# Kernel tuning notes

Measured on AMD Instinct MI355X. Metric: run time of the kernel, lower is better.

## Reference

```python
import jax, jax.numpy as jnp
import numpy as np
from math import factorial, comb

N_NODES = 50000
N_EDGES = 640000
FEAT = 32
NUM_BASIS = 8
CUTOFF = 5.0
MAX_Z = 118
NUM_ITERS = 3
LMAX = 2
K = (LMAX + 1) ** 2  # 9 spherical channels for max_degree=2


def _assoc_legendre(c, s, lmax):
    # associated Legendre P_l^m without Condon-Shortley phase
    P = {(0, 0): np.ones_like(c)}
    for m in range(1, lmax + 1):
        P[(m, m)] = P[(m - 1, m - 1)] * (2 * m - 1) * s
    for m in range(lmax):
        P[(m + 1, m)] = (2 * m + 1) * c * P[(m, m)]
    for m in range(lmax + 1):
        for l in range(m + 2, lmax + 1):
            P[(l, m)] = ((2 * l - 1) * c * P[(l - 1, m)] - (l + m - 1) * P[(l - 2, m)]) / (l - m)
    return P


def _real_sh_np(xyz, lmax):
    # Racah-normalized real spherical harmonics (Y_00 = 1), order m=-l..l
    r = np.linalg.norm(xyz, axis=1)
    cth = xyz[:, 2] / r
    sth = np.sqrt(np.maximum(1.0 - cth ** 2, 0.0))
    phi = np.arctan2(xyz[:, 1], xyz[:, 0])
    P = _assoc_legendre(cth, sth, lmax)
    cols = []
    for l in range(lmax + 1):
        for m in range(-l, l + 1):
            am = abs(m)
            if m == 0:
                cols.append(P[(l, 0)])
            else:
                nrm = np.sqrt(2.0 * factorial(l - am) / factorial(l + am))
                ang = np.cos(am * phi) if m > 0 else np.sin(am * phi)
                cols.append(nrm * P[(l, am)] * ang)
    return np.stack(cols, axis=1)


def _gaunt_tensor():
    # cg[k1,k2,k3]: expansion of Y_k1 * Y_k2 onto Y_k3 (degrees <= 2).
    # Products of degree<=2 harmonics lie exactly in span of degree<=4 harmonics,
    # so the least-squares fit below recovers exact coefficients.
    rng = np.random.default_rng(0)
    pts = rng.normal(size=(4096, 3))
    pts /= np.linalg.norm(pts, axis=1, keepdims=True)
    A = _real_sh_np(pts, 2 * LMAX)  # (M, 25)
    Y = A[:, :K]                    # (M, 9)
    prod = (Y[:, :, None] * Y[:, None, :]).reshape(len(pts), K * K)
    coef, *_ = np.linalg.lstsq(A, prod, rcond=None)  # (25, 81)
    return coef[:K].reshape(K, K, K).transpose(1, 2, 0).astype(np.float32)


CG = jnp.asarray(_gaunt_tensor())  # (9, 9, 9)
LOG_BINOM = jnp.asarray([np.log(comb(NUM_BASIS - 1, kk)) for kk in range(NUM_BASIS)], dtype=jnp.float32)


def _sh_l2(u):
    # Racah real SH of unit vectors, degrees 0..2, order m=-l..l
    x, y, z = u[:, 0], u[:, 1], u[:, 2]
    s3 = 1.7320508075688772
    return jnp.stack([
        jnp.ones_like(x),
        y, z, x,
        s3 * x * y, s3 * y * z, 0.5 * (3.0 * z * z - 1.0), s3 * x * z, 0.5 * s3 * (x * x - y * y),
    ], axis=1)


def _radial(r):
    # reciprocal Bernstein basis (log-space, stable) * smooth cutoff
    u = r / (1.0 + r)
    k = jnp.arange(NUM_BASIS, dtype=jnp.float32)
    n = float(NUM_BASIS - 1)
    eps = 1e-12
    logu = jnp.log(jnp.maximum(u, eps))[:, None]
    log1u = jnp.log(jnp.maximum(1.0 - u, eps))[:, None]
    bern = jnp.exp(LOG_BINOM + k * logu + (n - k) * log1u)  # (E, B)
    cut = jnp.where(r < CUTOFF, jnp.exp(-(r * r) / jnp.maximum(CUTOFF * CUTOFF - r * r, eps)), 0.0)
    return bern * cut[:, None]


def _forward(dr_vec, embed, rad_w, d1w, d1b, d2w, d2b, Z, neighbor_idxs):
    idx_i, idx_j = neighbor_idxs[0], neighbor_idxs[1]
    r = jnp.linalg.norm(dr_vec, axis=1)
    u = dr_vec / jnp.maximum(r, 1e-9)[:, None]
    Ysh = _sh_l2(u)              # (E, 9) angular basis
    rad = _radial(r)             # (E, B) radial basis
    # mask padding edges (idx_i == idx_j) as in mask_by_neighbor
    rad = rad * (idx_i != idx_j).astype(rad.dtype)[:, None]

    N = Z.shape[0]
    x = jnp.zeros((N, K, FEAT), jnp.float32).at[:, 0, :].set(embed[Z])

    for i in range(NUM_ITERS):
        last = i == NUM_ITERS - 1
        k3 = 1 if last else K    # last MessagePass has max_degree=0
        xe = x[idx_j]                                  # (E, 9, F) edge gather
        g = jnp.einsum('eb,dbf->edf', rad, rad_w[i])   # (E, 3, F) radial->feature per basis degree
        y = jnp.zeros((N_EDGES, k3, FEAT), jnp.float32)
        for l2 in range(LMAX + 1):
            sl = slice(l2 * l2, (l2 + 1) ** 2)
            c = jnp.einsum('abc,eb->eac', CG[:, sl, :k3], Ysh[:, sl])          # (E, 9, k3)
            y = y + jnp.einsum('eac,eaf->ecf', c, xe * g[:, l2][:, None, :])   # (E, k3, F)
        m = jax.ops.segment_sum(y, idx_i, num_segments=N)                      # scatter-sum
        if last:
            x = x[:, :1, :]      # change_max_degree_or_type(x, 0)
        h = x + m
        h = jnp.einsum('nkf,fg->nkg', h, d1w[i]).at[:, 0, :].add(d1b[i])
        gate = jax.nn.sigmoid(h[:, :1, :])
        h = h * gate             # silu on scalar channel, sigmoid-gated tensor channels
        h = jnp.einsum('nkf,fg->nkg', h, d2w[i]).at[:, 0, :].add(d2b[i])
        x = x + h
    return x[:, 0, :]            # (N, F)


def setup_inputs() -> dict:
    key = jax.random.key(0)
    ks = jax.random.split(key, 8)
    dr_vec = jax.random.normal(ks[0], (N_EDGES, 3), jnp.float32) * 2.0
    Z = jax.random.randint(ks[1], (N_NODES,), 0, MAX_Z + 1, jnp.int32)
    neighbor_idxs = jax.random.randint(ks[2], (2, N_EDGES), 0, N_NODES, jnp.int32)
    embed = jax.random.normal(ks[3], (MAX_Z + 1, FEAT), jnp.float32)
    rad_w = jax.random.normal(ks[4], (NUM_ITERS, LMAX + 1, NUM_BASIS, FEAT), jnp.float32) * 0.5
    d1w = jax.random.normal(ks[5], (NUM_ITERS, FEAT, FEAT), jnp.float32) * (1.0 / np.sqrt(FEAT))
    d1b = jnp.zeros((NUM_ITERS, FEAT), jnp.float32)
    d2w = jax.random.normal(ks[6], (NUM_ITERS, FEAT, FEAT), jnp.float32) * 0.02
    d2b = jnp.zeros((NUM_ITERS, FEAT), jnp.float32)
    return {"dr_vec": dr_vec, "embed": embed, "rad_w": rad_w, "d1w": d1w, "d1b": d1b,
            "d2w": d2w, "d2b": d2b, "Z": Z, "neighbor_idxs": neighbor_idxs}


def reference(dr_vec, embed, rad_w, d1w, d1b, d2w, d2b, Z, neighbor_idxs):
    return _forward(dr_vec, embed, rad_w, d1w, d1b, d2w, d2b, Z, neighbor_idxs)
```

## Files before the change

### kernel.cpp

```cpp
#include <hip/hip_runtime.h>
#include <hip/hip_fp16.h>
#include <math.h>

#define NN 50000
#define NE 640000
#define F  32
#define KCH 9
#define CUT 5.0f

#define C13 (1.0f/3.0f)
#define C23 (2.0f/3.0f)
#define C15 0.2f
#define C25 0.4f
#define C17 (1.0f/7.0f)
#define C27 (2.0f/7.0f)
#define IS3 0.5773502691896258f
#define S35 0.3464101615137755f
#define S37 0.2474358296526968f
#define S3  1.7320508075688772f

union U2H { unsigned int u; __half2 h; };

__device__ __forceinline__ unsigned int pack2(float a, float b) {
    U2H c; c.h = __floats2half2_rn(a, b); return c.u;
}
__device__ __forceinline__ float2 unpack2(unsigned int u) {
    U2H c; c.u = u; return __half22float2(c.h);
}
__device__ __forceinline__ float h2f(ushort u) {
    return __half2float(__ushort_as_half(u));
}

__global__ __launch_bounds__(256) void init_x(const float* __restrict__ embed,
                                              const int* __restrict__ Z,
                                              float* __restrict__ x0,
                                              ushort* __restrict__ x0h,
                                              uint4* __restrict__ xhA,
                                              ushort* __restrict__ xhB) {
    int idx = blockIdx.x * 256 + threadIdx.x;
    int n = idx >> 5, f = idx & 31;
    float v = embed[Z[n] * F + f];
    x0[idx] = v;
    unsigned int p = pack2(v, 0.f);
    x0h[idx] = (ushort)(p & 0xFFFFu);
    uint4 ua; ua.x = p; ua.y = 0u; ua.z = 0u; ua.w = 0u;
    xhA[idx] = ua;
    xhB[idx] = 0;
}

__global__ __launch_bounds__(256) void hist_kernel(const int* __restrict__ idx_i,
                                                   const int* __restrict__ idx_j,
                                                   const float* __restrict__ dr,
                                                   int* __restrict__ cnt) {
    int e = blockIdx.x * 256 + threadIdx.x;
    if (e >= NE) return;
    int ni = idx_i[e], nj = idx_j[e];
    float dx = dr[3 * e + 0], dy = dr[3 * e + 1], dz = dr[3 * e + 2];
    float r2 = fmaf(dx, dx, fmaf(dy, dy, dz * dz));
    if (ni != nj && r2 < CUT * CUT) atomicAdd(&cnt[ni], 1);
}

#define SCAN_T 1024
#define SCAN_C ((NN + SCAN_T - 1) / SCAN_T)

__global__ __launch_bounds__(SCAN_T) void scan_kernel(const int* __restrict__ cnt,
                                                      int* __restrict__ offs,
                                                      int* __restrict__ head) {
    __shared__ int ps[SCAN_T];
    int t = threadIdx.x;
    int b = t * SCAN_C;
    int e = min(b + SCAN_C, NN);
    int s = 0;
    for (int i = b; i < e; ++i) s += cnt[i];
    ps[t] = s;
    __syncthreads();
    for (int off = 1; off < SCAN_T; off <<= 1) {
        int v = (t >= off) ? ps[t - off] : 0;
        __syncthreads();
        ps[t] += v;
        __syncthreads();
    }
    int run = (t == 0) ? 0 : ps[t - 1];
    for (int i = b; i < e; ++i) { int c = cnt[i]; offs[i] = run; head[i] = run; run += c; }
    if (t == SCAN_T - 1) offs[NN] = ps[SCAN_T - 1];
}

__global__ __launch_bounds__(256) void fill_kernel(const int* __restrict__ idx_i,
                                                   const int* __restrict__ idx_j,
                                                   const float* __restrict__ dr,
                                                   int* __restrict__ head,
                                                   uint2* __restrict__ erec) {
    int e = blockIdx.x * 256 + threadIdx.x;
    if (e >= NE) return;
    int ni = idx_i[e], nj = idx_j[e];
    float dx = dr[3 * e + 0], dy = dr[3 * e + 1], dz = dr[3 * e + 2];
    float r2 = fmaf(dx, dx, fmaf(dy, dy, dz * dz));
    if (!(ni != nj && r2 < CUT * CUT)) return;

    float r = sqrtf(r2);
    float inv = 1.0f / fmaxf(r, 1e-9f);
    float ux = dx * inv, uy = dy * inv, uz = dz * inv;

    float cut = expf(-r2 / fmaxf(CUT * CUT - r2, 1e-12f));
    float ur = r / (1.0f + r), vr = 1.0f - ur;
    float up2 = ur*ur, up3 = up2*ur, up4 = up3*ur, up5 = up4*ur, up6 = up5*ur, up7 = up6*ur;
    float vp2 = vr*vr, vp3 = vp2*vr, vp4 = vp3*vr, vp5 = vp4*vr, vp6 = vp5*vr, vp7 = vp6*vr;

    float rc0 = cut * vp7;
    float rc1 = cut * 7.f  * ur  * vp6;
    float rc2 = cut * 21.f * up2 * vp5;
    float rc3 = cut * 35.f * up3 * vp4;
    float rc4 = cut * 35.f * up4 * vp3;
    float rc5 = cut * 21.f * up5 * vp2;
    float rc6 = cut * 7.f  * up6 * vr;
    float rc7 = cut * up7;

    int p = atomicAdd(&head[ni], 1);
    uint2 e0, e1, e2;
    U2H zh; zh.h = __floats2half2_rn(uz, 0.f);
    e0.x = pack2(ux, uy);
    e0.y = (zh.u & 0xFFFFu) | ((unsigned int)nj << 16);
    e1.x = pack2(rc0, rc1); e1.y = pack2(rc2, rc3);
    e2.x = pack2(rc4, rc5); e2.y = pack2(rc6, rc7);
    erec[(size_t)3 * p + 0] = e0;
    erec[(size_t)3 * p + 1] = e1;
    erec[(size_t)3 * p + 2] = e2;
}

template<int MODE>
__global__ __launch_bounds__(256) void gather_kernel(const uint2* __restrict__ erec,
                                                     const ushort* __restrict__ x0h,
                                                     const uint4* __restrict__ xhA,
                                                     const ushort* __restrict__ xhB,
                                                     const float* __restrict__ rw_iter,
                                                     const int* __restrict__ offs,
                                                     float* __restrict__ m) {
    const int NWAVES = 2048 * 4;
    int lane = threadIdx.x & 63;
    int wid  = threadIdx.x >> 6;
    int half = lane >> 5;
    int f    = lane & 31;
    int gw   = blockIdx.x * 4 + wid;

    float rwv[24];
    #pragma unroll
    for (int lb = 0; lb < 24; ++lb) rwv[lb] = rw_iter[lb * F + f];
    if (MODE == 2) {
        #pragma unroll
        for (int lb = 8; lb < 16; ++lb) rwv[lb] *= C13;
        #pragma unroll
        for (int lb = 16; lb < 24; ++lb) rwv[lb] *= C15;
    }

    constexpr int NACC = (MODE == 2) ? 1 : KCH;

    for (int n = gw; n < NN; n += NWAVES) {
        int start = offs[n], end = offs[n + 1];

        float acc[NACC];
        #pragma unroll
        for (int a = 0; a < NACC; ++a) acc[a] = 0.f;

        int t = start + half;
        uint2 e0_0 = {}, e0_1 = {}, e0_2 = {};
        uint4 xa_0 = {}, xa_1 = {};
        ushort x8_0 = 0, x8_1 = 0;

        if (t < end) {
            int c1 = min(t + 2, end - 1);
            int c2 = min(t + 4, end - 1);
            e0_0 = erec[(size_t)3 * t];
            e0_1 = erec[(size_t)3 * c1];
            e0_2 = erec[(size_t)3 * c2];
            int nj0 = (int)(e0_0.y >> 16);
            int nj1 = (int)(e0_1.y >> 16);
            if (MODE == 0) {
                x8_0 = x0h[nj0 * F + f];
                x8_1 = x0h[nj1 * F + f];
            } else {
                xa_0 = xhA[nj0 * F + f]; x8_0 = xhB[nj0 * F + f];
                xa_1 = xhA[nj1 * F + f]; x8_1 = xhB[nj1 * F + f];
            }
        }

        while (t < end) {
            uint2 e1 = erec[(size_t)3 * t + 1];
            uint2 e2 = erec[(size_t)3 * t + 2];

            int c3 = min(t + 6, end - 1);
            uint2 e0_3 = erec[(size_t)3 * c3];
            int nj2 = (int)(e0_2.y >> 16);
            uint4 xa_2 = {};
            ushort x8_2;
            if (MODE == 0) {
                x8_2 = x0h[nj2 * F + f];
            } else {
                xa_2 = xhA[nj2 * F + f];
                x8_2 = xhB[nj2 * F + f];
            }

            float2 uxy = unpack2(e0_0.x);
            float ux = uxy.x, uy = uxy.y;
            float uz = unpack2(e0_0.y).x;
            float2 rcA = unpack2(e1.x);
            float2 rcB = unpack2(e1.y);
            float2 rcC = unpack2(e2.x);
            float2 rcD = unpack2(e2.y);

            float g0, g1, g2;
            g0 = rcA.x * rwv[0];
            g0 = fmaf(rcA.y, rwv[1], g0); g0 = fmaf(rcB.x, rwv[2], g0); g0 = fmaf(rcB.y, rwv[3], g0);
            g0 = fmaf(rcC.x, rwv[4], g0); g0 = fmaf(rcC.y, rwv[5], g0); g0 = fmaf(rcD.x, rwv[6], g0);
            g0 = fmaf(rcD.y, rwv[7], g0);
            g1 = rcA.x * rwv[8];
            g1 = fmaf(rcA.y, rwv[9],  g1); g1 = fmaf(rcB.x, rwv[10], g1); g1 = fmaf(rcB.y, rwv[11], g1);
            g1 = fmaf(rcC.x, rwv[12], g1); g1 = fmaf(rcC.y, rwv[13], g1); g1 = fmaf(rcD.x, rwv[14], g1);
            g1 = fmaf(rcD.y, rwv[15], g1);
            g2 = rcA.x * rwv[16];
            g2 = fmaf(rcA.y, rwv[17], g2); g2 = fmaf(rcB.x, rwv[18], g2); g2 = fmaf(rcB.y, rwv[19], g2);
            g2 = fmaf(rcC.x, rwv[20], g2); g2 = fmaf(rcC.y, rwv[21], g2); g2 = fmaf(rcD.x, rwv[22], g2);
            g2 = fmaf(rcD.y, rwv[23], g2);

            if (MODE == 0) {
                float xe0 = h2f(x8_0);
                float s2 = S3 * g2;
                acc[0] = fmaf(xe0, g0, acc[0]);
                acc[1] = fmaf(xe0, uy * g1, acc[1]);
                acc[2] = fmaf(xe0, uz * g1, acc[2]);
                acc[3] = fmaf(xe0, ux * g1, acc[3]);
                acc[4] = fmaf(xe0, s2 * ux * uy, acc[4]);
                acc[5] = fmaf(xe0, s2 * uy * uz, acc[5]);
                acc[6] = fmaf(xe0, fmaf(1.5f * uz, uz, -0.5f) * g2, acc[6]);
                acc[7] = fmaf(xe0, s2 * ux * uz, acc[7]);
                acc[8] = fmaf(xe0, 0.5f * s2 * (ux * ux - uy * uy), acc[8]);
            } else {
                float xe[9];
                {
                    float2 p;
                    p = unpack2(xa_0.x); xe[0] = p.x; xe[1] = p.y;
                    p = unpack2(xa_0.y); xe[2] = p.x; xe[3] = p.y;
                    p = unpack2(xa_0.z); xe[4] = p.x; xe[5] = p.y;
                    p = unpack2(xa_0.w); xe[6] = p.x; xe[7] = p.y;
                    xe[8] = h2f(x8_0);
                }
                if (MODE == 2) {
                    float dot1 = uy * xe[1];
                    dot1 = fmaf(uz, xe[2], dot1);
                    dot1 = fmaf(ux, xe[3], dot1);
                    float Y4 = S3 * ux * uy, Y5 = S3 * uy * uz, Y7 = S3 * ux * uz;
                    float Y6 = fmaf(1.5f * uz, uz, -0.5f);
                    float Y8 = 0.5f * S3 * (ux * ux - uy * uy);
                    float dot2 = Y4 * xe[4];
                    dot2 = fmaf(Y5, xe[5], dot2);
                    dot2 = fmaf(Y6, xe[6], dot2);
                    dot2 = fmaf(Y7, xe[7], dot2);
                    dot2 = fmaf(Y8, xe[8], dot2);
                    acc[0] = fmaf(g0, xe[0], acc[0]);
                    acc[0] = fmaf(g1, dot1, acc[0]);
                    acc[0] = fmaf(g2, dot2, acc[0]);
                } else {
                    float s2 = S3 * g2;
                    float w[9];
                    w[0] = g0;
                    w[1] = uy * g1; w[2] = uz * g1; w[3] = ux * g1;
                    w[4] = s2 * ux * uy;
                    w[5] = s2 * uy * uz;
                    w[6] = fmaf(1.5f * uz, uz, -0.5f) * g2;
                    w[7] = s2 * ux * uz;
                    w[8] = 0.5f * s2 * (ux * ux - uy * uy);

                    float d0 = xe[0]*w[0], d1 = xe[1]*w[1], d2 = xe[2]*w[2], d3 = xe[3]*w[3];
                    float d4 = xe[4]*w[4], d5 = xe[5]*w[5], d6 = xe[6]*w[6], d7 = xe[7]*w[7];
                    float d8 = xe[8]*w[8];

                    acc[0] += d0 + C13 * (d1 + d2 + d3) + C15 * (d4 + d5 + d6 + d7 + d8);
                    #define T(a, b) (xe[a] * w[b] + xe[b] * w[a])
                    acc[1] += T(0,1) - C15 * T(1,6) - S35 * T(1,8) + S35 * T(2,5) + S35 * T(3,4);
                    acc[2] += T(0,2) + S35 * T(1,5) + C25 * T(2,6) + S35 * T(3,7);
                    acc[3] += T(0,3) + S35 * T(1,4) + S35 * T(2,7) - C15 * T(3,6) + S35 * T(3,8);
                    acc[4] += T(0,4) + IS3 * T(1,3) - C27 * T(4,6) + S37 * T(5,7);
                    acc[5] += T(0,5) + IS3 * T(1,2) + S37 * T(4,7) + C17 * T(5,6) - S37 * T(5,8);
                    acc[6] += T(0,6) - C13 * d1 + C23 * d2 - C13 * d3
                            - C27 * d4 + C17 * d5 + C27 * d6 + C17 * d7 - C27 * d8;
                    acc[7] += T(0,7) + IS3 * T(2,3) + S37 * T(4,5) + C17 * T(6,7) + S37 * T(7,8);
                    acc[8] += T(0,8) - IS3 * d1 + IS3 * d3 - S37 * d5 + S37 * d7 - C27 * T(6,8);
                    #undef T
                }
            }

            e0_0 = e0_1; e0_1 = e0_2; e0_2 = e0_3;
            xa_0 = xa_1; xa_1 = xa_2;
            x8_0 = x8_1; x8_1 = x8_2;
            t += 2;
        }

        #pragma unroll
        for (int a = 0; a < NACC; ++a) acc[a] += __shfl_xor(acc[a], 32);

        if (half == 0) {
            if (MODE == 2) {
                m[(size_t)n * F + f] = acc[0];
            } else {
                float* mp = m + (size_t)n * KCH * F + f;
                #pragma unroll
                for (int a = 0; a < KCH; ++a) mp[a * F] = acc[a];
            }
        }
    }
}

__global__ __launch_bounds__(256) void node_full(float* __restrict__ x0,
                                                 const float* __restrict__ m,
                                                 uint4* __restrict__ xhA,
                                                 ushort* __restrict__ xhB,
                                                 const float* __restrict__ w1,
                                                 const float* __restrict__ b1,
                                                 const float* __restrict__ w2,
                                                 const float* __restrict__ b2) {
    __shared__ float tile[8][KCH][F];
    int nl = threadIdx.x >> 5, f = threadIdx.x & 31;
    int n = blockIdx.x * 8 + nl;

    float w1c[F];
    #pragma unroll
    for (int fi = 0; fi < F; ++fi) w1c[fi] = w1[fi * F + f];

    float xk[KCH];
    {
        uint4 ua = xhA[n * F + f];
        ushort ub = xhB[n * F + f];
        float2 p;
        p = unpack2(ua.x); xk[0] = p.x; xk[1] = p.y;
        p = unpack2(ua.y); xk[2] = p.x; xk[3] = p.y;
        p = unpack2(ua.z); xk[4] = p.x; xk[5] = p.y;
        p = unpack2(ua.w); xk[6] = p.x; xk[7] = p.y;
        xk[8] = h2f(ub);
    }
    xk[0] = x0[n * F + f];

    #pragma unroll
    for (int k = 0; k < KCH; ++k)
        tile[nl][k][f] = xk[k] + m[((size_t)n * KCH + k) * F + f];
    __syncthreads();

    float o1[KCH];
    #pragma unroll
    for (int k = 0; k < KCH; ++k) {
        float s = 0.f;
        #pragma unroll
        for (int fi = 0; fi < F; ++fi) s = fmaf(tile[nl][k][fi], w1c[fi], s);
        o1[k] = s;
    }
    o1[0] += b1[f];
    float gate = 1.0f / (1.0f + expf(-o1[0]));
    __syncthreads();
    #pragma unroll
    for (int k = 0; k < KCH; ++k) tile[nl][k][f] = o1[k] * gate;
    __syncthreads();

    float w2c[F];
    #pragma unroll
    for (int fi = 0; fi < F; ++fi) w2c[fi] = w2[fi * F + f];

    float xn[KCH];
    #pragma unroll
    for (int k = 0; k < KCH; ++k) {
        float s = (k == 0) ? b2[f] : 0.f;
        #pragma unroll
        for (int fi = 0; fi < F; ++fi) s = fmaf(tile[nl][k][fi], w2c[fi], s);
        xn[k] = xk[k] + s;
    }

    x0[n * F + f] = xn[0];
    uint4 ua;
    ua.x = pack2(xn[0], xn[1]); ua.y = pack2(xn[2], xn[3]);
    ua.z = pack2(xn[4], xn[5]); ua.w = pack2(xn[6], xn[7]);
    xhA[n * F + f] = ua;
    xhB[n * F + f] = __half_as_ushort(__float2half_rn(xn[8]));
}

__global__ __launch_bounds__(256) void node_last(const float* __restrict__ x0,
                                                 const float* __restrict__ m1,
                                                 const float* __restrict__ w1,
                                                 const float* __restrict__ b1,
                                                 const float* __restrict__ w2,
                                                 const float* __restrict__ b2,
                                                 float* __restrict__ out) {
    __shared__ float tile[8][F];
    int nl = threadIdx.x >> 5, f = threadIdx.x & 31;
    int n = blockIdx.x * 8 + nl;

    float w1c[F];
    #pragma unroll
    for (int fi = 0; fi < F; ++fi) w1c[fi] = w1[fi * F + f];

    float xv = x0[n * F + f];
    tile[nl][f] = xv + m1[(size_t)n * F + f];
    __syncthreads();
    float s = 0.f;
    #pragma unroll
    for (int fi = 0; fi < F; ++fi) s = fmaf(tile[nl][fi], w1c[fi], s);
    s += b1[f];
    float gate = 1.0f / (1.0f + expf(-s));
    float h2 = s * gate;
    __syncthreads();
    tile[nl][f] = h2;
    __syncthreads();
    float w2c[F];
    #pragma unroll
    for (int fi = 0; fi < F; ++fi) w2c[fi] = w2[fi * F + f];
    float o = b2[f];
    #pragma unroll
    for (int fi = 0; fi < F; ++fi) o = fmaf(tile[nl][fi], w2c[fi], o);
    out[(size_t)n * F + f] = xv + o;
}

extern "C" void kernel_launch(void* const* d_in, const int* in_sizes, int n_in,
                              void* d_out, int out_size, void* d_ws, size_t ws_size,
                              hipStream_t stream) {
    (void)in_sizes; (void)n_in; (void)out_size; (void)ws_size;
    const float* dr    = (const float*)d_in[0];
    const float* embed = (const float*)d_in[1];
    const float* rad_w = (const float*)d_in[2];
    const float* d1w   = (const float*)d_in[3];
    const float* d1b   = (const float*)d_in[4];
    const float* d2w   = (const float*)d_in[5];
    const float* d2b   = (const float*)d_in[6];
    const int*   Z     = (const int*)d_in[7];
    const int*   nidx  = (const int*)d_in[8];
    const int* idx_i = nidx;
    const int* idx_j = nidx + NE;

    uint4* xhA = (uint4*)d_ws;
    float* m   = (float*)(xhA + (size_t)NN * F);
    float* x0  = m + (size_t)NN * KCH * F;
    ushort* x0h = (ushort*)(x0 + (size_t)NN * F);
    ushort* xhB = x0h + (size_t)NN * F;
    uint2* erec = (uint2*)(xhB + (size_t)NN * F);
    int* offs = (int*)(erec + (size_t)3 * NE);
    int* head = offs + (NN + 1);
    int* cnt  = head + NN;
    float* outp = (float*)d_out;

    hipMemsetAsync(cnt, 0, NN * sizeof(int), stream);
    hist_kernel<<<(NE + 255) / 256, 256, 0, stream>>>(idx_i, idx_j, dr, cnt);
    scan_kernel<<<1, SCAN_T, 0, stream>>>(cnt, offs, head);
    fill_kernel<<<(NE + 255) / 256, 256, 0, stream>>>(idx_i, idx_j, dr, head, erec);

    init_x<<<NN * F / 256, 256, 0, stream>>>(embed, Z, x0, x0h, xhA, xhB);

    for (int i = 0; i < 3; ++i) {
        const float* rwi = rad_w + (size_t)i * 3 * 8 * F;
        const float* w1 = d1w + (size_t)i * F * F;
        const float* b1 = d1b + (size_t)i * F;
        const float* w2 = d2w + (size_t)i * F * F;
        const float* b2 = d2b + (size_t)i * F;
        if (i == 0) {
            gather_kernel<0><<<2048, 256, 0, stream>>>(erec, x0h, xhA, xhB, rwi, offs, m);
            node_full<<<NN / 8, 256, 0, stream>>>(x0, m, xhA, xhB, w1, b1, w2, b2);
        } else if (i == 1) {
            gather_kernel<1><<<2048, 256, 0, stream>>>(erec, x0h, xhA, xhB, rwi, offs, m);
            node_full<<<NN / 8, 256, 0, stream>>>(x0, m, xhA, xhB, w1, b1, w2, b2);
        } else {
            gather_kernel<2><<<2048, 256, 0, stream>>>(erec, x0h, xhA, xhB, rwi, offs, m);
            node_last<<<NN / 8, 256, 0, stream>>>(x0, m, w1, b1, w2, b2, outp);
        }
    }
}
```

Measured before the change: 571.2 us.

## Split gather work into equal edge ranges with segmented atomic flushes

The gather kernel no longer assigns one node per wave. Each half-wave now takes an equal contiguous slice of the sorted edge list, accumulates per destination node, and flushes partial sums with float atomics whenever the destination changes. Edge records are repacked from three uint2 reads into a uint4 plus uint2 per edge, with a separate 16-bit destination array. The message buffer is zeroed before each iteration. The aim is even load balance and no idle lanes on low-degree nodes, paid for by an extra memset and atomic traffic at segment boundaries.

```diff
diff --git a/kernel.cpp b/kernel.cpp
--- a/kernel.cpp
+++ b/kernel.cpp
@@ -19,6 +19,9 @@
 #define S37 0.2474358296526968f
 #define S3  1.7320508075688772f
 
+#define NBLK 2048
+#define NHALF (NBLK * 8)
+
 union U2H { unsigned int u; __half2 h; };
 
 __device__ __forceinline__ unsigned int pack2(float a, float b) {
@@ -38,8 +41,8 @@
                                               uint4* __restrict__ xhA,
                                               ushort* __restrict__ xhB) {
     int idx = blockIdx.x * 256 + threadIdx.x;
-    int n = idx >> 5, f = idx & 31;
-    float v = embed[Z[n] * F + f];
+    int n = idx >> 5;
+    float v = embed[Z[n] * F + (idx & 31)];
     x0[idx] = v;
     unsigned int p = pack2(v, 0.f);
     x0h[idx] = (ushort)(p & 0xFFFFu);
@@ -89,7 +92,9 @@
                                                    const int* __restrict__ idx_j,
                                                    const float* __restrict__ dr,
                                                    int* __restrict__ head,
-                                                   uint2* __restrict__ erec) {
+                                                   uint4* __restrict__ geoA,
+                                                   uint2* __restrict__ geoB,
+                                                   ushort* __restrict__ dstA) {
     int e = blockIdx.x * 256 + threadIdx.x;
     if (e >= NE) return;
     int ni = idx_i[e], nj = idx_j[e];
@@ -106,41 +111,36 @@
     float up2 = ur*ur, up3 = up2*ur, up4 = up3*ur, up5 = up4*ur, up6 = up5*ur, up7 = up6*ur;
     float vp2 = vr*vr, vp3 = vp2*vr, vp4 = vp3*vr, vp5 = vp4*vr, vp6 = vp5*vr, vp7 = vp6*vr;
 
-    float rc0 = cut * vp7;
-    float rc1 = cut * 7.f  * ur  * vp6;
-    float rc2 = cut * 21.f * up2 * vp5;
-    float rc3 = cut * 35.f * up3 * vp4;
-    float rc4 = cut * 35.f * up4 * vp3;
-    float rc5 = cut * 21.f * up5 * vp2;
-    float rc6 = cut * 7.f  * up6 * vr;
-    float rc7 = cut * up7;
-
     int p = atomicAdd(&head[ni], 1);
-    uint2 e0, e1, e2;
+    uint4 gA;
     U2H zh; zh.h = __floats2half2_rn(uz, 0.f);
-    e0.x = pack2(ux, uy);
-    e0.y = (zh.u & 0xFFFFu) | ((unsigned int)nj << 16);
-    e1.x = pack2(rc0, rc1); e1.y = pack2(rc2, rc3);
-    e2.x = pack2(rc4, rc5); e2.y = pack2(rc6, rc7);
-    erec[(size_t)3 * p + 0] = e0;
-    erec[(size_t)3 * p + 1] = e1;
-    erec[(size_t)3 * p + 2] = e2;
+    gA.x = pack2(ux, uy);
+    gA.y = (zh.u & 0xFFFFu) | ((unsigned int)nj << 16);
+    gA.z = pack2(cut * vp7,        cut * 7.f  * ur  * vp6);
+    gA.w = pack2(cut * 21.f * up2 * vp5, cut * 35.f * up3 * vp4);
+    uint2 gB;
+    gB.x = pack2(cut * 35.f * up4 * vp3, cut * 21.f * up5 * vp2);
+    gB.y = pack2(cut * 7.f  * up6 * vr,  cut * up7);
+    geoA[p] = gA;
+    geoB[p] = gB;
+    dstA[p] = (ushort)ni;
 }
 
 template<int MODE>
-__global__ __launch_bounds__(256) void gather_kernel(const uint2* __restrict__ erec,
+__global__ __launch_bounds__(256) void gather_kernel(const uint4* __restrict__ geoA,
+                                                     const uint2* __restrict__ geoB,
+                                                     const ushort* __restrict__ dstA,
                                                      const ushort* __restrict__ x0h,
                                                      const uint4* __restrict__ xhA,
                                                      const ushort* __restrict__ xhB,
                                                      const float* __restrict__ rw_iter,
-                                                     const int* __restrict__ offs,
+                                                     const int* __restrict__ neptr,
                                                      float* __restrict__ m) {
-    const int NWAVES = 2048 * 4;
     int lane = threadIdx.x & 63;
     int wid  = threadIdx.x >> 6;
     int half = lane >> 5;
     int f    = lane & 31;
-    int gw   = blockIdx.x * 4 + wid;
+    int h    = blockIdx.x * 8 + wid * 2 + half;
 
     float rwv[24];
     #pragma unroll
@@ -152,159 +152,167 @@
         for (int lb = 16; lb < 24; ++lb) rwv[lb] *= C15;
     }
 
+    int NEl = neptr[0];
+    int per = (NEl + NHALF - 1) / NHALF;
+    int s = h * per;
+    int e = min(s + per, NEl);
+    if (s >= e) return;
+
     constexpr int NACC = (MODE == 2) ? 1 : KCH;
-
-    for (int n = gw; n < NN; n += NWAVES) {
-        int start = offs[n], end = offs[n + 1];
-
-        float acc[NACC];
-        #pragma unroll
-        for (int a = 0; a < NACC; ++a) acc[a] = 0.f;
-
-        int t = start + half;
-        uint2 e0_0 = {}, e0_1 = {}, e0_2 = {};
-        uint4 xa_0 = {}, xa_1 = {};
-        ushort x8_0 = 0, x8_1 = 0;
-
-        if (t < end) {
-            int c1 = min(t + 2, end - 1);
-            int c2 = min(t + 4, end - 1);
-            e0_0 = erec[(size_t)3 * t];
-            e0_1 = erec[(size_t)3 * c1];
-            e0_2 = erec[(size_t)3 * c2];
-            int nj0 = (int)(e0_0.y >> 16);
-            int nj1 = (int)(e0_1.y >> 16);
-            if (MODE == 0) {
-                x8_0 = x0h[nj0 * F + f];
-                x8_1 = x0h[nj1 * F + f];
+    float acc[NACC];
+    #pragma unroll
+    for (int a = 0; a < NACC; ++a) acc[a] = 0.f;
+    int cur = -1;
+
+    int c1 = min(s + 1, e - 1), c2 = min(s + 2, e - 1);
+    uint4 gA0 = geoA[s], gA1 = geoA[c1], gA2 = geoA[c2];
+    uint2 gB0 = geoB[s], gB1 = geoB[c1];
+    int d0 = dstA[s], d1 = dstA[c1];
+    int nj0 = (int)(gA0.y >> 16), nj1 = (int)(gA1.y >> 16);
+    uint4 xa0 = {}, xa1 = {};
+    ushort x80, x81;
+    if (MODE == 0) {
+        x80 = x0h[nj0 * F + f];
+        x81 = x0h[nj1 * F + f];
+    } else {
+        xa0 = xhA[nj0 * F + f]; x80 = xhB[nj0 * F + f];
+        xa1 = xhA[nj1 * F + f]; x81 = xhB[nj1 * F + f];
+    }
+
+    for (int t = s; t < e; ++t) {
+        int t3 = min(t + 3, e - 1);
+        int t2 = min(t + 2, e - 1);
+        uint4 gA3 = geoA[t3];
+        uint2 gB2 = geoB[t2];
+        int d2 = dstA[t2];
+        int nj2 = (int)(gA2.y >> 16);
+        uint4 xa2 = {};
+        ushort x82;
+        if (MODE == 0) {
+            x82 = x0h[nj2 * F + f];
+        } else {
+            xa2 = xhA[nj2 * F + f];
+            x82 = xhB[nj2 * F + f];
+        }
+
+        if (d0 != cur) {
+            if (cur >= 0) {
+                if (MODE == 2) {
+                    unsafeAtomicAdd(m + (size_t)cur * F + f, acc[0]);
+                } else {
+                    float* mp = m + (size_t)cur * KCH * F + f;
+                    #pragma unroll
+                    for (int a = 0; a < KCH; ++a) unsafeAtomicAdd(mp + a * F, acc[a]);
+                }
+            }
+            cur = d0;
+            #pragma unroll
+            for (int a = 0; a < NACC; ++a) acc[a] = 0.f;
+        }
+
+        float2 uxy = unpack2(gA0.x);
+        float ux = uxy.x, uy = uxy.y;
+        float uz = unpack2(gA0.y).x;
+        float2 rcA = unpack2(gA0.z);
+        float2 rcB = unpack2(gA0.w);
+        float2 rcC = unpack2(gB0.x);
+        float2 rcD = unpack2(gB0.y);
+
+        float g0, g1, g2;
+        g0 = rcA.x * rwv[0];
+        g0 = fmaf(rcA.y, rwv[1], g0); g0 = fmaf(rcB.x, rwv[2], g0); g0 = fmaf(rcB.y, rwv[3], g0);
+        g0 = fmaf(rcC.x, rwv[4], g0); g0 = fmaf(rcC.y, rwv[5], g0); g0 = fmaf(rcD.x, rwv[6], g0);
+        g0 = fmaf(rcD.y, rwv[7], g0);
+        g1 = rcA.x * rwv[8];
+        g1 = fmaf(rcA.y, rwv[9],  g1); g1 = fmaf(rcB.x, rwv[10], g1); g1 = fmaf(rcB.y, rwv[11], g1);
+        g1 = fmaf(rcC.x, rwv[12], g1); g1 = fmaf(rcC.y, rwv[13], g1); g1 = fmaf(rcD.x, rwv[14], g1);
+        g1 = fmaf(rcD.y, rwv[15], g1);
+        g2 = rcA.x * rwv[16];
+        g2 = fmaf(rcA.y, rwv[17], g2); g2 = fmaf(rcB.x, rwv[18], g2); g2 = fmaf(rcB.y, rwv[19], g2);
+        g2 = fmaf(rcC.x, rwv[20], g2); g2 = fmaf(rcC.y, rwv[21], g2); g2 = fmaf(rcD.x, rwv[22], g2);
+        g2 = fmaf(rcD.y, rwv[23], g2);
+
+        if (MODE == 0) {
+            float xe0 = h2f(x80);
+            float s2 = S3 * g2;
+            acc[0] = fmaf(xe0, g0, acc[0]);
+            acc[1] = fmaf(xe0, uy * g1, acc[1]);
+            acc[2] = fmaf(xe0, uz * g1, acc[2]);
+            acc[3] = fmaf(xe0, ux * g1, acc[3]);
+            acc[4] = fmaf(xe0, s2 * ux * uy, acc[4]);
+            acc[5] = fmaf(xe0, s2 * uy * uz, acc[5]);
+            acc[6] = fmaf(xe0, fmaf(1.5f * uz, uz, -0.5f) * g2, acc[6]);
+            acc[7] = fmaf(xe0, s2 * ux * uz, acc[7]);
+            acc[8] = fmaf(xe0, 0.5f * s2 * (ux * ux - uy * uy), acc[8]);
+        } else {
+            float xe[9];
+            {
+                float2 p;
+                p = unpack2(xa0.x); xe[0] = p.x; xe[1] = p.y;
+                p = unpack2(xa0.y); xe[2] = p.x; xe[3] = p.y;
+                p = unpack2(xa0.z); xe[4] = p.x; xe[5] = p.y;
+                p = unpack2(xa0.w); xe[6] = p.x; xe[7] = p.y;
+                xe[8] = h2f(x80);
+            }
+            if (MODE == 2) {
+                float dot1 = uy * xe[1];
+                dot1 = fmaf(uz, xe[2], dot1);
+                dot1 = fmaf(ux, xe[3], dot1);
+                float Y4 = S3 * ux * uy, Y5 = S3 * uy * uz, Y7 = S3 * ux * uz;
+                float Y6 = fmaf(1.5f * uz, uz, -0.5f);
+                float Y8 = 0.5f * S3 * (ux * ux - uy * uy);
+                float dot2 = Y4 * xe[4];
+                dot2 = fmaf(Y5, xe[5], dot2);
+                dot2 = fmaf(Y6, xe[6], dot2);
+                dot2 = fmaf(Y7, xe[7], dot2);
+                dot2 = fmaf(Y8, xe[8], dot2);
+                acc[0] = fmaf(g0, xe[0], acc[0]);
+                acc[0] = fmaf(g1, dot1, acc[0]);
+                acc[0] = fmaf(g2, dot2, acc[0]);
             } else {
-                xa_0 = xhA[nj0 * F + f]; x8_0 = xhB[nj0 * F + f];
-                xa_1 = xhA[nj1 * F + f]; x8_1 = xhB[nj1 * F + f];
+                float s2 = S3 * g2;
+                float w[9];
+                w[0] = g0;
+                w[1] = uy * g1; w[2] = uz * g1; w[3] = ux * g1;
+                w[4] = s2 * ux * uy;
+                w[5] = s2 * uy * uz;
+                w[6] = fmaf(1.5f * uz, uz, -0.5f) * g2;
+                w[7] = s2 * ux * uz;
+                w[8] = 0.5f * s2 * (ux * ux - uy * uy);
+
+                float d0v = xe[0]*w[0], d1v = xe[1]*w[1], d2v = xe[2]*w[2], d3v = xe[3]*w[3];
+                float d4v = xe[4]*w[4], d5v = xe[5]*w[5], d6v = xe[6]*w[6], d7v = xe[7]*w[7];
+                float d8v = xe[8]*w[8];
+
+                acc[0] += d0v + C13 * (d1v + d2v + d3v) + C15 * (d4v + d5v + d6v + d7v + d8v);
+                #define T(a, b) (xe[a] * w[b] + xe[b] * w[a])
+                acc[1] += T(0,1) - C15 * T(1,6) - S35 * T(1,8) + S35 * T(2,5) + S35 * T(3,4);
+                acc[2] += T(0,2) + S35 * T(1,5) + C25 * T(2,6) + S35 * T(3,7);
+                acc[3] += T(0,3) + S35 * T(1,4) + S35 * T(2,7) - C15 * T(3,6) + S35 * T(3,8);
+                acc[4] += T(0,4) + IS3 * T(1,3) - C27 * T(4,6) + S37 * T(5,7);
+                acc[5] += T(0,5) + IS3 * T(1,2) + S37 * T(4,7) + C17 * T(5,6) - S37 * T(5,8);
+                acc[6] += T(0,6) - C13 * d1v + C23 * d2v - C13 * d3v
+                        - C27 * d4v + C17 * d5v + C27 * d6v + C17 * d7v - C27 * d8v;
+                acc[7] += T(0,7) + IS3 * T(2,3) + S37 * T(4,5) + C17 * T(6,7) + S37 * T(7,8);
+                acc[8] += T(0,8) - IS3 * d1v + IS3 * d3v - S37 * d5v + S37 * d7v - C27 * T(6,8);
+                #undef T
             }
         }
 
-        while (t < end) {
-            uint2 e1 = erec[(size_t)3 * t + 1];
-            uint2 e2 = erec[(size_t)3 * t + 2];
-
-            int c3 = min(t + 6, end - 1);
-            uint2 e0_3 = erec[(size_t)3 * c3];
-            int nj2 = (int)(e0_2.y >> 16);
-            uint4 xa_2 = {};
-            ushort x8_2;
-            if (MODE == 0) {
-                x8_2 = x0h[nj2 * F + f];
-            } else {
-                xa_2 = xhA[nj2 * F + f];
-                x8_2 = xhB[nj2 * F + f];
-            }
-
-            float2 uxy = unpack2(e0_0.x);
-            float ux = uxy.x, uy = uxy.y;
-            float uz = unpack2(e0_0.y).x;
-            float2 rcA = unpack2(e1.x);
-            float2 rcB = unpack2(e1.y);
-            float2 rcC = unpack2(e2.x);
-            float2 rcD = unpack2(e2.y);
-
-            float g0, g1, g2;
-            g0 = rcA.x * rwv[0];
-            g0 = fmaf(rcA.y, rwv[1], g0); g0 = fmaf(rcB.x, rwv[2], g0); g0 = fmaf(rcB.y, rwv[3], g0);
-            g0 = fmaf(rcC.x, rwv[4], g0); g0 = fmaf(rcC.y, rwv[5], g0); g0 = fmaf(rcD.x, rwv[6], g0);
-            g0 = fmaf(rcD.y, rwv[7], g0);
-            g1 = rcA.x * rwv[8];
-            g1 = fmaf(rcA.y, rwv[9],  g1); g1 = fmaf(rcB.x, rwv[10], g1); g1 = fmaf(rcB.y, rwv[11], g1);
-            g1 = fmaf(rcC.x, rwv[12], g1); g1 = fmaf(rcC.y, rwv[13], g1); g1 = fmaf(rcD.x, rwv[14], g1);
-            g1 = fmaf(rcD.y, rwv[15], g1);
-            g2 = rcA.x * rwv[16];
-            g2 = fmaf(rcA.y, rwv[17], g2); g2 = fmaf(rcB.x, rwv[18], g2); g2 = fmaf(rcB.y, rwv[19], g2);
-            g2 = fmaf(rcC.x, rwv[20], g2); g2 = fmaf(rcC.y, rwv[21], g2); g2 = fmaf(rcD.x, rwv[22], g2);
-            g2 = fmaf(rcD.y, rwv[23], g2);
-
-            if (MODE == 0) {
-                float xe0 = h2f(x8_0);
-                float s2 = S3 * g2;
-                acc[0] = fmaf(xe0, g0, acc[0]);
-                acc[1] = fmaf(xe0, uy * g1, acc[1]);
-                acc[2] = fmaf(xe0, uz * g1, acc[2]);
-                acc[3] = fmaf(xe0, ux * g1, acc[3]);
-                acc[4] = fmaf(xe0, s2 * ux * uy, acc[4]);
-                acc[5] = fmaf(xe0, s2 * uy * uz, acc[5]);
-                acc[6] = fmaf(xe0, fmaf(1.5f * uz, uz, -0.5f) * g2, acc[6]);
-                acc[7] = fmaf(xe0, s2 * ux * uz, acc[7]);
-                acc[8] = fmaf(xe0, 0.5f * s2 * (ux * ux - uy * uy), acc[8]);
-            } else {
-                float xe[9];
-                {
-                    float2 p;
-                    p = unpack2(xa_0.x); xe[0] = p.x; xe[1] = p.y;
-                    p = unpack2(xa_0.y); xe[2] = p.x; xe[3] = p.y;
-                    p = unpack2(xa_0.z); xe[4] = p.x; xe[5] = p.y;
-                    p = unpack2(xa_0.w); xe[6] = p.x; xe[7] = p.y;
-                    xe[8] = h2f(x8_0);
-                }
-                if (MODE == 2) {
-                    float dot1 = uy * xe[1];
-                    dot1 = fmaf(uz, xe[2], dot1);
-                    dot1 = fmaf(ux, xe[3], dot1);
-                    float Y4 = S3 * ux * uy, Y5 = S3 * uy * uz, Y7 = S3 * ux * uz;
-                    float Y6 = fmaf(1.5f * uz, uz, -0.5f);
-                    float Y8 = 0.5f * S3 * (ux * ux - uy * uy);
-                    float dot2 = Y4 * xe[4];
-                    dot2 = fmaf(Y5, xe[5], dot2);
-                    dot2 = fmaf(Y6, xe[6], dot2);
-                    dot2 = fmaf(Y7, xe[7], dot2);
-                    dot2 = fmaf(Y8, xe[8], dot2);
-                    acc[0] = fmaf(g0, xe[0], acc[0]);
-                    acc[0] = fmaf(g1, dot1, acc[0]);
-                    acc[0] = fmaf(g2, dot2, acc[0]);
-                } else {
-                    float s2 = S3 * g2;
-                    float w[9];
-                    w[0] = g0;
-                    w[1] = uy * g1; w[2] = uz * g1; w[3] = ux * g1;
-                    w[4] = s2 * ux * uy;
-                    w[5] = s2 * uy * uz;
-                    w[6] = fmaf(1.5f * uz, uz, -0.5f) * g2;
-                    w[7] = s2 * ux * uz;
-                    w[8] = 0.5f * s2 * (ux * ux - uy * uy);
-
-                    float d0 = xe[0]*w[0], d1 = xe[1]*w[1], d2 = xe[2]*w[2], d3 = xe[3]*w[3];
-                    float d4 = xe[4]*w[4], d5 = xe[5]*w[5], d6 = xe[6]*w[6], d7 = xe[7]*w[7];
-                    float d8 = xe[8]*w[8];
-
-                    acc[0] += d0 + C13 * (d1 + d2 + d3) + C15 * (d4 + d5 + d6 + d7 + d8);
-                    #define T(a, b) (xe[a] * w[b] + xe[b] * w[a])
-                    acc[1] += T(0,1) - C15 * T(1,6) - S35 * T(1,8) + S35 * T(2,5) + S35 * T(3,4);
-                    acc[2] += T(0,2) + S35 * T(1,5) + C25 * T(2,6) + S35 * T(3,7);
-                    acc[3] += T(0,3) + S35 * T(1,4) + S35 * T(2,7) - C15 * T(3,6) + S35 * T(3,8);
-                    acc[4] += T(0,4) + IS3 * T(1,3) - C27 * T(4,6) + S37 * T(5,7);
-                    acc[5] += T(0,5) + IS3 * T(1,2) + S37 * T(4,7) + C17 * T(5,6) - S37 * T(5,8);
-                    acc[6] += T(0,6) - C13 * d1 + C23 * d2 - C13 * d3
-                            - C27 * d4 + C17 * d5 + C27 * d6 + C17 * d7 - C27 * d8;
-                    acc[7] += T(0,7) + IS3 * T(2,3) + S37 * T(4,5) + C17 * T(6,7) + S37 * T(7,8);
-                    acc[8] += T(0,8) - IS3 * d1 + IS3 * d3 - S37 * d5 + S37 * d7 - C27 * T(6,8);
-                    #undef T
-                }
-            }
-
-            e0_0 = e0_1; e0_1 = e0_2; e0_2 = e0_3;
-            xa_0 = xa_1; xa_1 = xa_2;
-            x8_0 = x8_1; x8_1 = x8_2;
-            t += 2;
-        }
-
-        #pragma unroll
-        for (int a = 0; a < NACC; ++a) acc[a] += __shfl_xor(acc[a], 32);
-
-        if (half == 0) {
-            if (MODE == 2) {
-                m[(size_t)n * F + f] = acc[0];
-            } else {
-                float* mp = m + (size_t)n * KCH * F + f;
-                #pragma unroll
-                for (int a = 0; a < KCH; ++a) mp[a * F] = acc[a];
-            }
+        gA0 = gA1; gA1 = gA2; gA2 = gA3;
+        gB0 = gB1; gB1 = gB2;
+        d0 = d1; d1 = d2;
+        xa0 = xa1; xa1 = xa2;
+        x80 = x81; x81 = x82;
+    }
+
+    if (cur >= 0) {
+        if (MODE == 2) {
+            unsafeAtomicAdd(m + (size_t)cur * F + f, acc[0]);
+        } else {
+            float* mp = m + (size_t)cur * KCH * F + f;
+            #pragma unroll
+            for (int a = 0; a < KCH; ++a) unsafeAtomicAdd(mp + a * F, acc[a]);
         }
     }
 }
@@ -431,24 +439,30 @@
     const int* idx_i = nidx;
     const int* idx_j = nidx + NE;
 
-    uint4* xhA = (uint4*)d_ws;
-    float* m   = (float*)(xhA + (size_t)NN * F);
-    float* x0  = m + (size_t)NN * KCH * F;
+    uint4* xhA  = (uint4*)d_ws;
+    float* m    = (float*)(xhA + (size_t)NN * F);
+    float* x0   = m + (size_t)NN * KCH * F;
     ushort* x0h = (ushort*)(x0 + (size_t)NN * F);
     ushort* xhB = x0h + (size_t)NN * F;
-    uint2* erec = (uint2*)(xhB + (size_t)NN * F);
-    int* offs = (int*)(erec + (size_t)3 * NE);
+    uint4* geoA = (uint4*)(xhB + (size_t)NN * F);
+    uint2* geoB = (uint2*)(geoA + (size_t)NE);
+    ushort* dstA = (ushort*)(geoB + (size_t)NE);
+    int* offs = (int*)(dstA + (size_t)NE + 4);
     int* head = offs + (NN + 1);
     int* cnt  = head + NN;
     float* outp = (float*)d_out;
 
+    size_t MB_full = (size_t)NN * KCH * F * sizeof(float);
+    size_t MB_last = (size_t)NN * F * sizeof(float);
+
     hipMemsetAsync(cnt, 0, NN * sizeof(int), stream);
     hist_kernel<<<(NE + 255) / 256, 256, 0, stream>>>(idx_i, idx_j, dr, cnt);
     scan_kernel<<<1, SCAN_T, 0, stream>>>(cnt, offs, head);
-    fill_kernel<<<(NE + 255) / 256, 256, 0, stream>>>(idx_i, idx_j, dr, head, erec);
+    fill_kernel<<<(NE + 255) / 256, 256, 0, stream>>>(idx_i, idx_j, dr, head, geoA, geoB, dstA);
 
     init_x<<<NN * F / 256, 256, 0, stream>>>(embed, Z, x0, x0h, xhA, xhB);
 
+    const int* neptr = offs + NN;
     for (int i = 0; i < 3; ++i) {
         const float* rwi = rad_w + (size_t)i * 3 * 8 * F;
         const float* w1 = d1w + (size_t)i * F * F;
@@ -456,13 +470,16 @@
         const float* w2 = d2w + (size_t)i * F * F;
         const float* b2 = d2b + (size_t)i * F;
         if (i == 0) {
-            gather_kernel<0><<<2048, 256, 0, stream>>>(erec, x0h, xhA, xhB, rwi, offs, m);
+            hipMemsetAsync(m, 0, MB_full, stream);
+            gather_kernel<0><<<NBLK, 256, 0, stream>>>(geoA, geoB, dstA, x0h, xhA, xhB, rwi, neptr, m);
             node_full<<<NN / 8, 256, 0, stream>>>(x0, m, xhA, xhB, w1, b1, w2, b2);
         } else if (i == 1) {
-            gather_kernel<1><<<2048, 256, 0, stream>>>(erec, x0h, xhA, xhB, rwi, offs, m);
+            hipMemsetAsync(m, 0, MB_full, stream);
+            gather_kernel<1><<<NBLK, 256, 0, stream>>>(geoA, geoB, dstA, x0h, xhA, xhB, rwi, neptr, m);
             node_full<<<NN / 8, 256, 0, stream>>>(x0, m, xhA, xhB, w1, b1, w2, b2);
         } else {
-            gather_kernel<2><<<2048, 256, 0, stream>>>(erec, x0h, xhA, xhB, rwi, offs, m);
+            hipMemsetAsync(m, 0, MB_last, stream);
+            gather_kernel<2><<<NBLK, 256, 0, stream>>>(geoA, geoB, dstA, x0h, xhA, xhB, rwi, neptr, m);
             node_last<<<NN / 8, 256, 0, stream>>>(x0, m, w1, b1, w2, b2, outp);
         }
     }
```

Result: no change. 581.0 us (+1.7%).
